# Optimization experiments

Measured on AMD Instinct MI355X. Metric: run time of the kernel, lower is better.

## Reference

```python
import jax, jax.numpy as jnp
import numpy as np

D_MODEL = 128
NHEAD = 8
NLAYERS = 6
LAYER_NAMES = ['self', 'cross', 'self', 'cross', 'self', 'cross']
TEMPERATURE = 5.0
EPS = 1e-6


def _pos_encoding(x):
    # Sinusoidal 1D position encoding along the width axis. x: [N, H, W, C]
    C, W = x.shape[-1], x.shape[2]
    pos = jnp.arange(W, dtype=x.dtype)[:, None]                      # [W,1]
    div = jnp.exp(jnp.arange(0, C, 2, dtype=x.dtype) * (-np.log(10000.0) / C))
    pe = jnp.zeros((W, C), x.dtype)
    pe = pe.at[:, 0::2].set(jnp.sin(pos * div))
    pe = pe.at[:, 1::2].set(jnp.cos(pos * div))
    return x + pe[None, None]                                        # broadcast over N,H


def _linear_attention(q, k, v):
    # q,k,v: [N, H, W, nhead, dim]; kernelized linear attention along W
    Q = jax.nn.elu(q) + 1.0
    K = jax.nn.elu(k) + 1.0
    v_len = v.shape[2]
    V = v / v_len
    KV = jnp.einsum('nhsed,nhsev->nhedv', K, V)                      # [N,H,e,d,d]
    Z = 1.0 / (jnp.einsum('nhled,nhed->nhle', Q, K.sum(axis=2)) + EPS)
    return jnp.einsum('nhled,nhedv,nhle->nhlev', Q, KV, Z) * v_len


def _layer_norm(x, g, b):
    m = x.mean(-1, keepdims=True)
    v = jnp.mean((x - m) ** 2, -1, keepdims=True)
    return (x - m) / jnp.sqrt(v + 1e-5) * g + b


def _encoder_layer(x, source, Wq, Wk, Wv, Wm, W1, W2, g1, b1, g2, b2):
    x = _pos_encoding(x)
    source = _pos_encoding(source)
    bs, h, w, c = x.shape
    e, d = NHEAD, c // NHEAD
    q = (x @ Wq).reshape(bs, h, w, e, d)
    k = (source @ Wk).reshape(bs, h, w, e, d)
    v = (source @ Wv).reshape(bs, h, w, e, d)
    msg = _linear_attention(q, k, v).reshape(bs, h, w, c) @ Wm
    msg = _layer_norm(msg, g1, b1)
    msg = jnp.concatenate([x, msg], axis=-1)                         # [N,H,W,2C]
    msg = jax.nn.relu(msg @ W1) @ W2
    msg = _layer_norm(msg, g2, b2)
    return x + msg


def _forward(feat0, feat1, Wq, Wk, Wv, Wm, W1, W2, g1, b1, g2, b2):
    feat0 = feat0.transpose(0, 2, 3, 1)                              # [N,H,W,C]
    feat1 = feat1.transpose(0, 2, 3, 1)
    for i, name in enumerate(LAYER_NAMES):
        p = (Wq[i], Wk[i], Wv[i], Wm[i], W1[i], W2[i], g1[i], b1[i], g2[i], b2[i])
        if name == 'self':
            feat0 = _encoder_layer(feat0, feat0, *p)
            feat1 = _encoder_layer(feat1, feat1, *p)
        else:  # cross: sequential update (feat1 sees updated feat0), as in torch source
            feat0 = _encoder_layer(feat0, feat1, *p)
            feat1 = _encoder_layer(feat1, feat0, *p)
    w = feat0.shape[2]
    attn_mask = jnp.where(jnp.triu(jnp.ones((w, w), bool), 1), -jnp.inf, 0.0)
    attn_mask = attn_mask[None, None].astype(feat0.dtype)
    scale = feat0.shape[-1] ** 0.5
    sim = jnp.einsum('ntwc,ntlc->ntwl', feat0 / scale, feat1 / scale) / TEMPERATURE
    return sim + attn_mask


def setup_inputs() -> dict:
    key = jax.random.key(0)
    ks = jax.random.split(key, 12)
    N, C, H, W = 2, D_MODEL, 64, 640
    L, D = NLAYERS, D_MODEL
    s = 1.0 / np.sqrt(D)
    s2 = 1.0 / np.sqrt(2 * D)
    return {
        'feat0': jax.random.normal(ks[0], (N, C, H, W), jnp.float32),
        'feat1': jax.random.normal(ks[1], (N, C, H, W), jnp.float32),
        'Wq': jax.random.normal(ks[2], (L, D, D), jnp.float32) * s,
        'Wk': jax.random.normal(ks[3], (L, D, D), jnp.float32) * s,
        'Wv': jax.random.normal(ks[4], (L, D, D), jnp.float32) * s,
        'Wm': jax.random.normal(ks[5], (L, D, D), jnp.float32) * s,
        'W1': jax.random.normal(ks[6], (L, 2 * D, 2 * D), jnp.float32) * s2,
        'W2': jax.random.normal(ks[7], (L, 2 * D, D), jnp.float32) * s2,
        'g1': jnp.ones((L, D), jnp.float32),
        'b1': jnp.zeros((L, D), jnp.float32),
        'g2': jnp.ones((L, D), jnp.float32),
        'b2': jnp.zeros((L, D), jnp.float32),
    }


def reference(feat0, feat1, Wq, Wk, Wv, Wm, W1, W2, g1, b1, g2, b2):
    return _forward(feat0, feat1, Wq, Wk, Wv, Wm, W1, W2, g1, b1, g2, b2)
```

## Files before the change

### kernel.cpp

```cpp
#include <hip/hip_runtime.h>
#include <cmath>
#include <math.h>

#define TOK 81920
#define WDIM 640

typedef __attribute__((ext_vector_type(8))) short short8v;
typedef __attribute__((ext_vector_type(4))) float f32x4;

__device__ __forceinline__ short f2bf(float f) {
  union { float f; unsigned u; } x; x.f = f;
  unsigned r = (x.u + 0x7fffu + ((x.u >> 16) & 1u)) >> 16;
  return (short)r;
}
__device__ __forceinline__ float bf2f(short s) {
  union { unsigned u; float f; } x; x.u = ((unsigned)(unsigned short)s) << 16;
  return x.f;
}

__global__ __launch_bounds__(256) void pe_kernel(float* __restrict__ pe) {
  int id = blockIdx.x * 256 + threadIdx.x;
  if (id >= WDIM * 128) return;
  int w = id >> 7;
  int c = id & 127;
  float i2 = (float)(c & 126);
  float freq = expf(i2 * -0.071955784156063941f);
  float ang = (float)w * freq;
  pe[id] = (c & 1) ? cosf(ang) : sinf(ang);
}

__global__ __launch_bounds__(256) void tr_kernel(const float* __restrict__ in0,
                                                 const float* __restrict__ in1,
                                                 short* __restrict__ x0,
                                                 short* __restrict__ x1) {
  __shared__ float t[32][33];
  int w0 = blockIdx.x * 32;
  int c0 = blockIdx.y * 32;
  int z = blockIdx.z;
  int feat = z >> 7;
  int nh = z & 127;
  int n = nh >> 6, h = nh & 63;
  const float* in = feat ? in1 : in0;
  short* out = feat ? x1 : x0;
  int tx = threadIdx.x & 31, ty = threadIdx.x >> 5;
  const float* ip = in + ((n * 128 + c0) * 64 + h) * 640 + w0;
#pragma unroll
  for (int i = 0; i < 32; i += 8)
    t[ty + i][tx] = ip[(ty + i) * (64 * 640) + tx];
  __syncthreads();
  short* op = out + ((size_t)(n * 64 + h) * 640 + w0) * 128 + c0;
#pragma unroll
  for (int i = 0; i < 32; i += 8)
    op[(size_t)(ty + i) * 128 + tx] = f2bf(t[tx][ty + i]);
}

__global__ __launch_bounds__(256) void wprep_kernel(
    const float* __restrict__ Wq, const float* __restrict__ Wk,
    const float* __restrict__ Wv, const float* __restrict__ Wm,
    const float* __restrict__ W1, const float* __restrict__ W2,
    short* __restrict__ BT) {
  int id = blockIdx.x * 256 + threadIdx.x;
  if (id >= 6 * 163840) return;
  int layer = id / 163840;
  int r = id % 163840;
  float v;
  if (r < 65536) {
    int seg = r >> 14;
    int rr = r & 16383;
    int n = rr >> 7, k = rr & 127;
    const float* W = seg == 0 ? Wq : seg == 1 ? Wk : seg == 2 ? Wv : Wm;
    v = W[layer * 16384 + k * 128 + n];
  } else if (r < 131072) {
    int rr = r - 65536;
    int n = rr >> 8, k = rr & 255;
    v = W1[layer * 65536 + k * 256 + n];
  } else {
    int rr = r - 131072;
    int n = rr >> 8, k = rr & 255;
    v = W2[layer * 32768 + k * 128 + n];
  }
  BT[id] = f2bf(v);
}

__device__ __forceinline__ void load_af(const short* __restrict__ A,
                                        const float* __restrict__ pe,
                                        int bm, int wr, int l15, int lk,
                                        short8v af[4][4]) {
  const int wbase = bm % WDIM;
#pragma unroll
  for (int mf = 0; mf < 4; ++mf) {
    const int rl = wr * 64 + mf * 16 + l15;
    const short* ar = A + (size_t)(bm + rl) * 128;
    const float* pr = pe + (size_t)(wbase + rl) * 128;
#pragma unroll
    for (int ks = 0; ks < 4; ++ks) {
      const int kloc = ks * 32 + lk * 8;
      short8v xa = *(const short8v*)(ar + kloc);
      f32x4 p0 = *(const f32x4*)(pr + kloc);
      f32x4 p1 = *(const f32x4*)(pr + kloc + 4);
      short8v o;
      o[0] = f2bf(bf2f(xa[0]) + p0[0]); o[1] = f2bf(bf2f(xa[1]) + p0[1]);
      o[2] = f2bf(bf2f(xa[2]) + p0[2]); o[3] = f2bf(bf2f(xa[3]) + p0[3]);
      o[4] = f2bf(bf2f(xa[4]) + p1[0]); o[5] = f2bf(bf2f(xa[5]) + p1[1]);
      o[6] = f2bf(bf2f(xa[6]) + p1[2]); o[7] = f2bf(bf2f(xa[7]) + p1[3]);
      af[ks][mf] = o;
    }
  }
}

__device__ __forceinline__ void proj_pass(const short8v af[4][4],
                                          const short* __restrict__ WT,
                                          int bm, int wr, int wc, int l15, int lk,
                                          short* __restrict__ out) {
  f32x4 acc[4][4] = {};
#pragma unroll
  for (int ks = 0; ks < 4; ++ks) {
    const int kloc = ks * 32 + lk * 8;
    short8v bfr[4];
#pragma unroll
    for (int nf = 0; nf < 4; ++nf)
      bfr[nf] = *(const short8v*)&WT[(size_t)(wc * 64 + nf * 16 + l15) * 128 + kloc];
#pragma unroll
    for (int mf = 0; mf < 4; ++mf)
#pragma unroll
      for (int nf = 0; nf < 4; ++nf)
        acc[mf][nf] = __builtin_amdgcn_mfma_f32_16x16x32_bf16(
            af[ks][mf], bfr[nf], acc[mf][nf], 0, 0, 0);
  }
#pragma unroll
  for (int mf = 0; mf < 4; ++mf)
#pragma unroll
    for (int nf = 0; nf < 4; ++nf) {
      const int colL = wc * 64 + nf * 16 + l15;
#pragma unroll
      for (int r = 0; r < 4; ++r) {
        const int row = bm + wr * 64 + mf * 16 + lk * 4 + r;
        out[(size_t)row * 128 + colL] = f2bf(acc[mf][nf][r]);
      }
    }
}

__global__ __launch_bounds__(256) void qkv_self_kernel(
    const short* __restrict__ x0, const short* __restrict__ x1,
    const float* __restrict__ pe,
    const short* __restrict__ wqT, const short* __restrict__ wkT,
    const short* __restrict__ wvT,
    short* q0, short* k0, short* v0, short* q1, short* k1, short* v1) {
  const int tid = threadIdx.x, lane = tid & 63, wid = tid >> 6;
  const int wr = wid >> 1, wc = wid & 1;
  const int bm = blockIdx.x * 128;
  const int l15 = lane & 15, lk = lane >> 4;
  const int z = blockIdx.z;
  const short* A = z ? x1 : x0;
  short8v af[4][4];
  load_af(A, pe, bm, wr, l15, lk, af);
  proj_pass(af, wqT, bm, wr, wc, l15, lk, z ? q1 : q0);
  proj_pass(af, wkT, bm, wr, wc, l15, lk, z ? k1 : k0);
  proj_pass(af, wvT, bm, wr, wc, l15, lk, z ? v1 : v0);
}

__global__ __launch_bounds__(256) void qkv_cross_kernel(
    const short* __restrict__ xq, const short* __restrict__ xs,
    const float* __restrict__ pe,
    const short* __restrict__ wqT, const short* __restrict__ wkT,
    const short* __restrict__ wvT,
    short* qb, short* kb, short* vb) {
  const int tid = threadIdx.x, lane = tid & 63, wid = tid >> 6;
  const int wr = wid >> 1, wc = wid & 1;
  const int bm = blockIdx.x * 128;
  const int l15 = lane & 15, lk = lane >> 4;
  short8v af[4][4];
  if (blockIdx.y == 0) {
    load_af(xq, pe, bm, wr, l15, lk, af);
    proj_pass(af, wqT, bm, wr, wc, l15, lk, qb);
  } else {
    load_af(xs, pe, bm, wr, l15, lk, af);
    proj_pass(af, wkT, bm, wr, wc, l15, lk, kb);
    proj_pass(af, wvT, bm, wr, wc, l15, lk, vb);
  }
}

template <int NSC>
__global__ __launch_bounds__(256) void kv_kernel(
    const short* __restrict__ k0, const short* __restrict__ v0,
    const short* __restrict__ k1, const short* __restrict__ v1,
    float* __restrict__ kvp) {
  const int bid = blockIdx.x;
  const int sc = bid % NSC;
  const int e = bid / NSC;
  const int strip = sc / 5, chunk = sc % 5;
  const short* kb = (strip >= 128) ? k1 : k0;
  const short* vb = (strip >= 128) ? v1 : v0;
  const int nh = strip & 127;
  const size_t base = (size_t)nh * (640 * 128) + (size_t)chunk * (128 * 128) + e * 16;
  __shared__ float Ks[128][16];
  __shared__ float Vs[128][16];
  const int tid = threadIdx.x;
  const int srow = tid >> 1, shalf = (tid & 1) * 8;
  short8v k8 = *(const short8v*)&kb[base + (size_t)srow * 128 + shalf];
  short8v v8 = *(const short8v*)&vb[base + (size_t)srow * 128 + shalf];
#pragma unroll
  for (int j = 0; j < 8; ++j) {
    float kr = bf2f(k8[j]);
    Ks[srow][shalf + j] = kr > 0.f ? kr + 1.f : __expf(kr);
    Vs[srow][shalf + j] = bf2f(v8[j]);
  }
  __syncthreads();
  const int d = tid >> 4, vv = tid & 15;
  float kv = 0.f, ks = 0.f;
#pragma unroll 8
  for (int sl = 0; sl < 128; ++sl) {
    float kk = Ks[sl][d];
    kv = fmaf(kk, Vs[sl][vv], kv);
    ks += kk;
  }
  float* out = kvp + ((size_t)(strip * 8 + e) * 5 + chunk) * 272;
  out[d * 16 + vv] = kv;
  if (vv == 0) out[256 + d] = ks;
}

template <int DUAL>
__global__ __launch_bounds__(256) void apply_wm_kernel(
    short* q0, short* q1, const float* __restrict__ kvp,
    const short* __restrict__ wmT,
    const float* __restrict__ g, const float* __restrict__ b) {
  const int bid = blockIdx.x;
  const int strip = bid / 10, lc = bid % 10;
  __shared__ float KV8[8][16][17];
  __shared__ float KS8[8][16];
  __shared__ short oS[64][136];
  const int tid = threadIdx.x;
  for (int idx = tid; idx < 8 * 272; idx += 256) {
    int e = idx / 272, r = idx - e * 272;
    const float* p = kvp + ((size_t)(strip * 8 + e) * 5) * 272 + r;
    float s = ((p[0] + p[272]) + (p[544] + p[816])) + p[1088];
    if (r < 256) KV8[e][r >> 4][r & 15] = s;
    else         KS8[e][r - 256] = s;
  }
  __syncthreads();
  short* qb = (DUAL && strip >= 128) ? q1 : q0;
  const int nh = strip & 127;
  const int lrow = tid >> 2;
  const int row = lc * 64 + lrow;
  const int cb = (tid & 3) * 32;
  short* qp = qb + (size_t)nh * (640 * 128) + (size_t)row * 128 + cb;
  short8v qv0 = *(const short8v*)(qp);
  short8v qv1 = *(const short8v*)(qp + 8);
  short8v qv2 = *(const short8v*)(qp + 16);
  short8v qv3 = *(const short8v*)(qp + 24);
  float qe[32];
#pragma unroll
  for (int j = 0; j < 8; ++j) {
    float a = bf2f(qv0[j]); qe[j]      = a > 0.f ? a + 1.f : __expf(a);
    float c1 = bf2f(qv1[j]); qe[8 + j]  = c1 > 0.f ? c1 + 1.f : __expf(c1);
    float c2 = bf2f(qv2[j]); qe[16 + j] = c2 > 0.f ? c2 + 1.f : __expf(c2);
    float c3 = bf2f(qv3[j]); qe[24 + j] = c3 > 0.f ? c3 + 1.f : __expf(c3);
  }
  short res[32];
#pragma unroll
  for (int h = 0; h < 2; ++h) {
    const int e = (cb >> 4) + h;
    const float* Q = qe + h * 16;
    float dz = 0.f;
#pragma unroll
    for (int dd = 0; dd < 16; ++dd) dz = fmaf(Q[dd], KS8[e][dd], dz);
    const float zi = 1.f / (dz + 1e-6f);
#pragma unroll
    for (int vv = 0; vv < 16; ++vv) {
      float o = 0.f;
#pragma unroll
      for (int dd = 0; dd < 16; ++dd) o = fmaf(Q[dd], KV8[e][dd][vv], o);
      res[h * 16 + vv] = f2bf(o * zi);
    }
  }
  short8v w0, w1, w2, w3;
#pragma unroll
  for (int j = 0; j < 8; ++j) {
    w0[j] = res[j]; w1[j] = res[8 + j]; w2[j] = res[16 + j]; w3[j] = res[24 + j];
  }
  *(short8v*)&oS[lrow][cb]      = w0;
  *(short8v*)&oS[lrow][cb + 8]  = w1;
  *(short8v*)&oS[lrow][cb + 16] = w2;
  *(short8v*)&oS[lrow][cb + 24] = w3;
  __syncthreads();
  const int lane = tid & 63, w = tid >> 6;
  const int l15 = lane & 15, lk = lane >> 4;
  f32x4 acc[8] = {};
#pragma unroll
  for (int ks = 0; ks < 4; ++ks) {
    const int kloc = ks * 32 + lk * 8;
    short8v afr = *(const short8v*)&oS[w * 16 + l15][kloc];
    short8v bfr[8];
#pragma unroll
    for (int nf = 0; nf < 8; ++nf)
      bfr[nf] = *(const short8v*)&wmT[(size_t)(nf * 16 + l15) * 128 + kloc];
#pragma unroll
    for (int nf = 0; nf < 8; ++nf)
      acc[nf] = __builtin_amdgcn_mfma_f32_16x16x32_bf16(afr, bfr[nf], acc[nf], 0, 0, 0);
  }
  float gv[8], bv[8];
#pragma unroll
  for (int nf = 0; nf < 8; ++nf) { gv[nf] = g[nf * 16 + l15]; bv[nf] = b[nf * 16 + l15]; }
#pragma unroll
  for (int r = 0; r < 4; ++r) {
    float s = 0.f, qq = 0.f;
#pragma unroll
    for (int nf = 0; nf < 8; ++nf) {
      s += acc[nf][r];
      qq = fmaf(acc[nf][r], acc[nf][r], qq);
    }
#pragma unroll
    for (int off = 1; off < 16; off <<= 1) {
      s += __shfl_xor(s, off);
      qq += __shfl_xor(qq, off);
    }
    float mean = s * (1.f / 128.f);
    float var = qq * (1.f / 128.f) - mean * mean;
    float rstd = rsqrtf(var + 1e-5f);
    const int grow = lc * 64 + w * 16 + lk * 4 + r;
    short* mp = qb + (size_t)nh * (640 * 128) + (size_t)grow * 128;
#pragma unroll
    for (int nf = 0; nf < 8; ++nf)
      mp[nf * 16 + l15] = f2bf((acc[nf][r] - mean) * rstd * gv[nf] + bv[nf]);
  }
}

__global__ __launch_bounds__(256) void w1_kernel(
    const short* __restrict__ xA, const short* __restrict__ xB,
    const short* __restrict__ mA, const short* __restrict__ mB,
    const float* __restrict__ pe, const short* __restrict__ w1T,
    short* h0A, short* h1A, short* h0B, short* h1B) {
  const int z = blockIdx.z;
  const short* x = z ? xB : xA;
  const short* m = z ? mB : mA;
  short* h0 = z ? h0B : h0A;
  short* h1 = z ? h1B : h1A;
  const int tid = threadIdx.x, lane = tid & 63, wid = tid >> 6;
  const int wr = wid >> 1, wc = wid & 1;
  const int bm = blockIdx.x * 128;
  const int l15 = lane & 15, lk = lane >> 4;
  const int wbase = bm % WDIM;
  for (int p = 0; p < 2; ++p) {
    f32x4 acc[4][4] = {};
#pragma unroll
    for (int ks = 0; ks < 8; ++ks) {
      const int kloc = ks * 32 + lk * 8;
      short8v bfr[4], afr[4];
#pragma unroll
      for (int nf = 0; nf < 4; ++nf)
        bfr[nf] = *(const short8v*)&w1T[(size_t)(p * 128 + wc * 64 + nf * 16 + l15) * 256 + kloc];
      if (ks < 4) {
#pragma unroll
        for (int mf = 0; mf < 4; ++mf) {
          const int rl = wr * 64 + mf * 16 + l15;
          short8v xa = *(const short8v*)(x + (size_t)(bm + rl) * 128 + kloc);
          const float* pr = pe + (size_t)(wbase + rl) * 128 + kloc;
          f32x4 p0 = *(const f32x4*)pr;
          f32x4 p1 = *(const f32x4*)(pr + 4);
          short8v ov;
          ov[0] = f2bf(bf2f(xa[0]) + p0[0]); ov[1] = f2bf(bf2f(xa[1]) + p0[1]);
          ov[2] = f2bf(bf2f(xa[2]) + p0[2]); ov[3] = f2bf(bf2f(xa[3]) + p0[3]);
          ov[4] = f2bf(bf2f(xa[4]) + p1[0]); ov[5] = f2bf(bf2f(xa[5]) + p1[1]);
          ov[6] = f2bf(bf2f(xa[6]) + p1[2]); ov[7] = f2bf(bf2f(xa[7]) + p1[3]);
          afr[mf] = ov;
        }
      } else {
#pragma unroll
        for (int mf = 0; mf < 4; ++mf)
          afr[mf] = *(const short8v*)&m[(size_t)(bm + wr * 64 + mf * 16 + l15) * 128 + kloc - 128];
      }
#pragma unroll
      for (int mf = 0; mf < 4; ++mf)
#pragma unroll
        for (int nf = 0; nf < 4; ++nf)
          acc[mf][nf] = __builtin_amdgcn_mfma_f32_16x16x32_bf16(
              afr[mf], bfr[nf], acc[mf][nf], 0, 0, 0);
    }
    short* h = p ? h1 : h0;
#pragma unroll
    for (int mf = 0; mf < 4; ++mf)
#pragma unroll
      for (int nf = 0; nf < 4; ++nf) {
        const int colL = wc * 64 + nf * 16 + l15;
#pragma unroll
        for (int r = 0; r < 4; ++r) {
          const int row = bm + wr * 64 + mf * 16 + lk * 4 + r;
          h[(size_t)row * 128 + colL] = f2bf(fmaxf(acc[mf][nf][r], 0.f));
        }
      }
  }
}

__global__ __launch_bounds__(256) void w2_ln_kernel(
    const short* __restrict__ h0A, const short* __restrict__ h1A,
    const short* __restrict__ h0B, const short* __restrict__ h1B,
    const short* __restrict__ w2T, short* xA, short* xB,
    const float* __restrict__ pe, const float* __restrict__ g,
    const float* __restrict__ b) {
  const int z = blockIdx.z;
  const short* h0 = z ? h0B : h0A;
  const short* h1 = z ? h1B : h1A;
  short* x = z ? xB : xA;
  __shared__ float lds_s[2][128];
  __shared__ float lds_q[2][128];
  const int tid = threadIdx.x, lane = tid & 63, wid = tid >> 6;
  const int wr = wid >> 1, wc = wid & 1;
  const int bm = blockIdx.x * 128;
  const int l15 = lane & 15, lk = lane >> 4;
  const int wbase = bm % WDIM;
  f32x4 acc[4][4] = {};
#pragma unroll
  for (int ks = 0; ks < 8; ++ks) {
    const int kloc = ks * 32 + lk * 8;
    const short* hp = (ks < 4) ? h0 : h1;
    const int kl = (ks < 4) ? kloc : kloc - 128;
    short8v bfr[4], afr[4];
#pragma unroll
    for (int nf = 0; nf < 4; ++nf)
      bfr[nf] = *(const short8v*)&w2T[(size_t)(wc * 64 + nf * 16 + l15) * 256 + kloc];
#pragma unroll
    for (int mf = 0; mf < 4; ++mf)
      afr[mf] = *(const short8v*)&hp[(size_t)(bm + wr * 64 + mf * 16 + l15) * 128 + kl];
#pragma unroll
    for (int mf = 0; mf < 4; ++mf)
#pragma unroll
      for (int nf = 0; nf < 4; ++nf)
        acc[mf][nf] = __builtin_amdgcn_mfma_f32_16x16x32_bf16(
            afr[mf], bfr[nf], acc[mf][nf], 0, 0, 0);
  }
#pragma unroll
  for (int mf = 0; mf < 4; ++mf)
#pragma unroll
    for (int r = 0; r < 4; ++r) {
      float s = acc[mf][0][r] + acc[mf][1][r] + acc[mf][2][r] + acc[mf][3][r];
      float qq = acc[mf][0][r] * acc[mf][0][r] + acc[mf][1][r] * acc[mf][1][r]
               + acc[mf][2][r] * acc[mf][2][r] + acc[mf][3][r] * acc[mf][3][r];
#pragma unroll
      for (int off = 1; off < 16; off <<= 1) {
        s += __shfl_xor(s, off);
        qq += __shfl_xor(qq, off);
      }
      if (l15 == 0) {
        int rl = wr * 64 + mf * 16 + lk * 4 + r;
        lds_s[wc][rl] = s;
        lds_q[wc][rl] = qq;
      }
    }
  __syncthreads();
  float gv[4], bv[4];
#pragma unroll
  for (int nf = 0; nf < 4; ++nf) {
    int c = wc * 64 + nf * 16 + l15;
    gv[nf] = g[c]; bv[nf] = b[c];
  }
#pragma unroll
  for (int mf = 0; mf < 4; ++mf)
#pragma unroll
    for (int r = 0; r < 4; ++r) {
      int rl = wr * 64 + mf * 16 + lk * 4 + r;
      float mean = (lds_s[0][rl] + lds_s[1][rl]) * (1.f / 128.f);
      float var = (lds_q[0][rl] + lds_q[1][rl]) * (1.f / 128.f) - mean * mean;
      float rstd = rsqrtf(var + 1e-5f);
      int row = bm + rl;
#pragma unroll
      for (int nf = 0; nf < 4; ++nf) {
        int col = wc * 64 + nf * 16 + l15;
        float ln = (acc[mf][nf][r] - mean) * rstd * gv[nf] + bv[nf];
        size_t xi = (size_t)row * 128 + col;
        float xv = bf2f(x[xi]) + pe[(size_t)(wbase + rl) * 128 + col] + ln;
        x[xi] = f2bf(xv);
      }
    }
}

__global__ __launch_bounds__(256) void sim_mfma(const short* __restrict__ f0,
                                                const short* __restrict__ f1,
                                                float* __restrict__ out) {
  const int fid = (blockIdx.z * 5 + blockIdx.y) * 5 + blockIdx.x;
  const int c8 = fid & 7, kk_ = fid >> 3;
  const int nt = c8 * 16 + kk_ / 25;
  const int r2 = kk_ % 25;
  const int bw = (r2 % 5) * 128;
  const int bl = (r2 / 5) * 128;
  const int tid = threadIdx.x;
  const int lane = tid & 63;
  const int wid = tid >> 6;
  const int wr = wid >> 1, wc = wid & 1;
  const short* __restrict__ A = f0 + (size_t)nt * 640 * 128;
  const short* __restrict__ B = f1 + (size_t)nt * 640 * 128;
  const int l15 = lane & 15;
  const int lk = lane >> 4;
  f32x4 acc[4][4] = {};
#pragma unroll
  for (int ks = 0; ks < 4; ++ks) {
    const int kloc = ks * 32 + lk * 8;
    short8v afr[4], bfr[4];
#pragma unroll
    for (int mf = 0; mf < 4; ++mf)
      afr[mf] = *(const short8v*)&A[(size_t)(bw + wr * 64 + mf * 16 + l15) * 128 + kloc];
#pragma unroll
    for (int nf = 0; nf < 4; ++nf)
      bfr[nf] = *(const short8v*)&B[(size_t)(bl + wc * 64 + nf * 16 + l15) * 128 + kloc];
#pragma unroll
    for (int mf = 0; mf < 4; ++mf)
#pragma unroll
      for (int nf = 0; nf < 4; ++nf)
        acc[mf][nf] = __builtin_amdgcn_mfma_f32_16x16x32_bf16(
            afr[mf], bfr[nf], acc[mf][nf], 0, 0, 0);
  }
#pragma unroll
  for (int mf = 0; mf < 4; ++mf)
#pragma unroll
    for (int nf = 0; nf < 4; ++nf) {
      const int l = bl + wc * 64 + nf * 16 + l15;
#pragma unroll
      for (int r = 0; r < 4; ++r) {
        const int w = bw + wr * 64 + mf * 16 + lk * 4 + r;
        float v = acc[mf][nf][r] * (1.f / 640.f);
        if (l > w) v = -1e30f;
        out[((size_t)nt * 640 + w) * 640 + l] = v;
      }
    }
}

extern "C" void kernel_launch(void* const* d_in, const int* in_sizes, int n_in,
                              void* d_out, int out_size, void* d_ws, size_t ws_size,
                              hipStream_t stream) {
  (void)in_sizes; (void)n_in; (void)out_size; (void)ws_size;
  const float* feat0 = (const float*)d_in[0];
  const float* feat1 = (const float*)d_in[1];
  const float* Wq = (const float*)d_in[2];
  const float* Wk = (const float*)d_in[3];
  const float* Wv = (const float*)d_in[4];
  const float* Wm = (const float*)d_in[5];
  const float* W1 = (const float*)d_in[6];
  const float* W2 = (const float*)d_in[7];
  const float* g1 = (const float*)d_in[8];
  const float* b1 = (const float*)d_in[9];
  const float* g2 = (const float*)d_in[10];
  const float* b2 = (const float*)d_in[11];

  float* wsf = (float*)d_ws;
  const size_t U = (size_t)TOK * 128;
  float* pe = wsf;
  short* x0 = (short*)(wsf + 81920);
  short* x1 = x0 + U;
  short* q0 = x1 + U;
  short* k0 = q0 + U;
  short* v0 = k0 + U;
  short* q1 = v0 + U;
  short* k1 = q1 + U;
  short* v1 = k1 + U;
  short* bt = v1 + U;
  float* kvp = (float*)(bt + 983040);

  dim3 blk(256);
  pe_kernel<<<dim3(320), blk, 0, stream>>>(pe);
  tr_kernel<<<dim3(20, 4, 256), blk, 0, stream>>>(feat0, feat1, x0, x1);
  wprep_kernel<<<dim3((6 * 163840 + 255) / 256), blk, 0, stream>>>(
      Wq, Wk, Wv, Wm, W1, W2, bt);

  const int NB = TOK / 128;
  for (int i = 0; i < 6; ++i) {
    const short* bt_i = bt + (size_t)i * 163840;
    const short* wqT = bt_i;
    const short* wkT = bt_i + 16384;
    const short* wvT = bt_i + 32768;
    const short* wmT = bt_i + 49152;
    const short* w1T = bt_i + 65536;
    const short* w2T = bt_i + 131072;
    const float* g1_i = g1 + i * 128;
    const float* b1_i = b1 + i * 128;
    const float* g2_i = g2 + i * 128;
    const float* b2_i = b2 + i * 128;
    if ((i & 1) == 0) {
      qkv_self_kernel<<<dim3(NB, 1, 2), blk, 0, stream>>>(
          x0, x1, pe, wqT, wkT, wvT, q0, k0, v0, q1, k1, v1);
      kv_kernel<1280><<<dim3(8 * 1280), blk, 0, stream>>>(k0, v0, k1, v1, kvp);
      apply_wm_kernel<1><<<dim3(2560), blk, 0, stream>>>(q0, q1, kvp, wmT, g1_i, b1_i);
      w1_kernel<<<dim3(NB, 1, 2), blk, 0, stream>>>(
          x0, x1, q0, q1, pe, w1T, k0, v0, k1, v1);
      w2_ln_kernel<<<dim3(NB, 1, 2), blk, 0, stream>>>(
          k0, v0, k1, v1, w2T, x0, x1, pe, g2_i, b2_i);
    } else {
      qkv_cross_kernel<<<dim3(NB, 2), blk, 0, stream>>>(
          x0, x1, pe, wqT, wkT, wvT, q0, k0, v0);
      kv_kernel<640><<<dim3(8 * 640), blk, 0, stream>>>(k0, v0, k0, v0, kvp);
      apply_wm_kernel<0><<<dim3(1280), blk, 0, stream>>>(q0, q0, kvp, wmT, g1_i, b1_i);
      w1_kernel<<<dim3(NB, 1, 1), blk, 0, stream>>>(
          x0, x0, q0, q0, pe, w1T, k0, v0, k0, v0);
      w2_ln_kernel<<<dim3(NB, 1, 1), blk, 0, stream>>>(
          k0, v0, k0, v0, w2T, x0, x0, pe, g2_i, b2_i);

      qkv_cross_kernel<<<dim3(NB, 2), blk, 0, stream>>>(
          x1, x0, pe, wqT, wkT, wvT, q0, k0, v0);
      kv_kernel<640><<<dim3(8 * 640), blk, 0, stream>>>(k0, v0, k0, v0, kvp);
      apply_wm_kernel<0><<<dim3(1280), blk, 0, stream>>>(q0, q0, kvp, wmT, g1_i, b1_i);
      w1_kernel<<<dim3(NB, 1, 1), blk, 0, stream>>>(
          x1, x1, q0, q0, pe, w1T, k0, v0, k0, v0);
      w2_ln_kernel<<<dim3(NB, 1, 1), blk, 0, stream>>>(
          k0, v0, k0, v0, w2T, x1, x1, pe, g2_i, b2_i);
    }
  }
  sim_mfma<<<dim3(5, 5, 128), blk, 0, stream>>>(x0, x1, (float*)d_out);
}
```

Baseline: 2.767 ms.

## Stage GEMM epilogues through LDS for coalesced 16-byte global stores

Swaps the MFMA operand order so each lane holds four contiguous output columns, packs them into short4 writes to a padded LDS tile, then writes the tile to global memory with coalesced 16-byte stores. This applies to the QKV projections, the attention-output/Wm LayerNorm epilogue, the W1 ReLU epilogue and the W2 LayerNorm-residual epilogue. It replaces scattered 2-byte strided global stores and simplifies the LayerNorm reductions to two cross-lane shuffles. In exchange it adds LDS usage and extra barriers per block, which may reduce occupancy.

```diff
diff --git a/kernel.cpp b/kernel.cpp
--- a/kernel.cpp
+++ b/kernel.cpp
@@ -6,6 +6,7 @@
 #define WDIM 640
 
 typedef __attribute__((ext_vector_type(8))) short short8v;
+typedef __attribute__((ext_vector_type(4))) short short4v;
 typedef __attribute__((ext_vector_type(4))) float f32x4;
 
 __device__ __forceinline__ short f2bf(float f) {
@@ -108,10 +109,10 @@
   }
 }
 
-__device__ __forceinline__ void proj_pass(const short8v af[4][4],
-                                          const short* __restrict__ WT,
-                                          int bm, int wr, int wc, int l15, int lk,
-                                          short* __restrict__ out) {
+__device__ __forceinline__ void proj_pass_T(const short8v af[4][4],
+                                            const short* __restrict__ WT,
+                                            int wr, int wc, int l15, int lk,
+                                            short (*tS)[136]) {
   f32x4 acc[4][4] = {};
 #pragma unroll
   for (int ks = 0; ks < 4; ++ks) {
@@ -125,19 +126,28 @@
 #pragma unroll
       for (int nf = 0; nf < 4; ++nf)
         acc[mf][nf] = __builtin_amdgcn_mfma_f32_16x16x32_bf16(
-            af[ks][mf], bfr[nf], acc[mf][nf], 0, 0, 0);
+            bfr[nf], af[ks][mf], acc[mf][nf], 0, 0, 0);
   }
 #pragma unroll
   for (int mf = 0; mf < 4; ++mf)
 #pragma unroll
     for (int nf = 0; nf < 4; ++nf) {
-      const int colL = wc * 64 + nf * 16 + l15;
-#pragma unroll
-      for (int r = 0; r < 4; ++r) {
-        const int row = bm + wr * 64 + mf * 16 + lk * 4 + r;
-        out[(size_t)row * 128 + colL] = f2bf(acc[mf][nf][r]);
-      }
-    }
+      short4v p;
+      p[0] = f2bf(acc[mf][nf][0]); p[1] = f2bf(acc[mf][nf][1]);
+      p[2] = f2bf(acc[mf][nf][2]); p[3] = f2bf(acc[mf][nf][3]);
+      *(short4v*)&tS[wr * 64 + mf * 16 + l15][wc * 64 + nf * 16 + lk * 4] = p;
+    }
+}
+
+__device__ __forceinline__ void tile_out(const short (*tS)[136], int bm, int tid,
+                                         short* __restrict__ out) {
+#pragma unroll
+  for (int it = 0; it < 8; ++it) {
+    int u = it * 256 + tid;
+    int row = u >> 4, seg = u & 15;
+    *(short8v*)&out[(size_t)(bm + row) * 128 + seg * 8] =
+        *(const short8v*)&tS[row][seg * 8];
+  }
 }
 
 __global__ __launch_bounds__(256) void qkv_self_kernel(
@@ -146,6 +156,7 @@
     const short* __restrict__ wqT, const short* __restrict__ wkT,
     const short* __restrict__ wvT,
     short* q0, short* k0, short* v0, short* q1, short* k1, short* v1) {
+  __shared__ short tS[128][136];
   const int tid = threadIdx.x, lane = tid & 63, wid = tid >> 6;
   const int wr = wid >> 1, wc = wid & 1;
   const int bm = blockIdx.x * 128;
@@ -154,9 +165,17 @@
   const short* A = z ? x1 : x0;
   short8v af[4][4];
   load_af(A, pe, bm, wr, l15, lk, af);
-  proj_pass(af, wqT, bm, wr, wc, l15, lk, z ? q1 : q0);
-  proj_pass(af, wkT, bm, wr, wc, l15, lk, z ? k1 : k0);
-  proj_pass(af, wvT, bm, wr, wc, l15, lk, z ? v1 : v0);
+  proj_pass_T(af, wqT, wr, wc, l15, lk, tS);
+  __syncthreads();
+  tile_out(tS, bm, tid, z ? q1 : q0);
+  __syncthreads();
+  proj_pass_T(af, wkT, wr, wc, l15, lk, tS);
+  __syncthreads();
+  tile_out(tS, bm, tid, z ? k1 : k0);
+  __syncthreads();
+  proj_pass_T(af, wvT, wr, wc, l15, lk, tS);
+  __syncthreads();
+  tile_out(tS, bm, tid, z ? v1 : v0);
 }
 
 __global__ __launch_bounds__(256) void qkv_cross_kernel(
@@ -165,6 +184,7 @@
     const short* __restrict__ wqT, const short* __restrict__ wkT,
     const short* __restrict__ wvT,
     short* qb, short* kb, short* vb) {
+  __shared__ short tS[128][136];
   const int tid = threadIdx.x, lane = tid & 63, wid = tid >> 6;
   const int wr = wid >> 1, wc = wid & 1;
   const int bm = blockIdx.x * 128;
@@ -172,11 +192,18 @@
   short8v af[4][4];
   if (blockIdx.y == 0) {
     load_af(xq, pe, bm, wr, l15, lk, af);
-    proj_pass(af, wqT, bm, wr, wc, l15, lk, qb);
+    proj_pass_T(af, wqT, wr, wc, l15, lk, tS);
+    __syncthreads();
+    tile_out(tS, bm, tid, qb);
   } else {
     load_af(xs, pe, bm, wr, l15, lk, af);
-    proj_pass(af, wkT, bm, wr, wc, l15, lk, kb);
-    proj_pass(af, wvT, bm, wr, wc, l15, lk, vb);
+    proj_pass_T(af, wkT, wr, wc, l15, lk, tS);
+    __syncthreads();
+    tile_out(tS, bm, tid, kb);
+    __syncthreads();
+    proj_pass_T(af, wvT, wr, wc, l15, lk, tS);
+    __syncthreads();
+    tile_out(tS, bm, tid, vb);
   }
 }
 
@@ -283,45 +310,51 @@
   *(short8v*)&oS[lrow][cb + 16] = w2;
   *(short8v*)&oS[lrow][cb + 24] = w3;
   __syncthreads();
-  const int lane = tid & 63, w = tid >> 6;
+  const int lane = tid & 63, wv = tid >> 6;
   const int l15 = lane & 15, lk = lane >> 4;
   f32x4 acc[8] = {};
 #pragma unroll
   for (int ks = 0; ks < 4; ++ks) {
     const int kloc = ks * 32 + lk * 8;
-    short8v afr = *(const short8v*)&oS[w * 16 + l15][kloc];
+    short8v afr = *(const short8v*)&oS[wv * 16 + l15][kloc];
     short8v bfr[8];
 #pragma unroll
     for (int nf = 0; nf < 8; ++nf)
       bfr[nf] = *(const short8v*)&wmT[(size_t)(nf * 16 + l15) * 128 + kloc];
 #pragma unroll
     for (int nf = 0; nf < 8; ++nf)
-      acc[nf] = __builtin_amdgcn_mfma_f32_16x16x32_bf16(afr, bfr[nf], acc[nf], 0, 0, 0);
-  }
-  float gv[8], bv[8];
-#pragma unroll
-  for (int nf = 0; nf < 8; ++nf) { gv[nf] = g[nf * 16 + l15]; bv[nf] = b[nf * 16 + l15]; }
-#pragma unroll
-  for (int r = 0; r < 4; ++r) {
-    float s = 0.f, qq = 0.f;
-#pragma unroll
-    for (int nf = 0; nf < 8; ++nf) {
+      acc[nf] = __builtin_amdgcn_mfma_f32_16x16x32_bf16(bfr[nf], afr, acc[nf], 0, 0, 0);
+  }
+  float s = 0.f, qq = 0.f;
+#pragma unroll
+  for (int nf = 0; nf < 8; ++nf)
+#pragma unroll
+    for (int r = 0; r < 4; ++r) {
       s += acc[nf][r];
       qq = fmaf(acc[nf][r], acc[nf][r], qq);
     }
-#pragma unroll
-    for (int off = 1; off < 16; off <<= 1) {
-      s += __shfl_xor(s, off);
-      qq += __shfl_xor(qq, off);
-    }
-    float mean = s * (1.f / 128.f);
-    float var = qq * (1.f / 128.f) - mean * mean;
-    float rstd = rsqrtf(var + 1e-5f);
-    const int grow = lc * 64 + w * 16 + lk * 4 + r;
-    short* mp = qb + (size_t)nh * (640 * 128) + (size_t)grow * 128;
-#pragma unroll
-    for (int nf = 0; nf < 8; ++nf)
-      mp[nf * 16 + l15] = f2bf((acc[nf][r] - mean) * rstd * gv[nf] + bv[nf]);
+  s += __shfl_xor(s, 16);  qq += __shfl_xor(qq, 16);
+  s += __shfl_xor(s, 32);  qq += __shfl_xor(qq, 32);
+  float mean = s * (1.f / 128.f);
+  float var = qq * (1.f / 128.f) - mean * mean;
+  float rstd = rsqrtf(var + 1e-5f);
+#pragma unroll
+  for (int nf = 0; nf < 8; ++nf) {
+    f32x4 g4 = *(const f32x4*)&g[nf * 16 + lk * 4];
+    f32x4 b4 = *(const f32x4*)&b[nf * 16 + lk * 4];
+    short4v p;
+#pragma unroll
+    for (int r = 0; r < 4; ++r)
+      p[r] = f2bf((acc[nf][r] - mean) * rstd * g4[r] + b4[r]);
+    *(short4v*)&oS[wv * 16 + l15][nf * 16 + lk * 4] = p;
+  }
+  __syncthreads();
+  short* mp = qb + (size_t)nh * (640 * 128) + (size_t)(lc * 64) * 128;
+#pragma unroll
+  for (int it = 0; it < 4; ++it) {
+    int u = it * 256 + tid;
+    int rw = u >> 4, seg = u & 15;
+    *(short8v*)&mp[(size_t)rw * 128 + seg * 8] = *(const short8v*)&oS[rw][seg * 8];
   }
 }
 
@@ -330,6 +363,7 @@
     const short* __restrict__ mA, const short* __restrict__ mB,
     const float* __restrict__ pe, const short* __restrict__ w1T,
     short* h0A, short* h1A, short* h0B, short* h1B) {
+  __shared__ short tS[128][136];
   const int z = blockIdx.z;
   const short* x = z ? xB : xA;
   const short* m = z ? mB : mA;
@@ -374,20 +408,21 @@
 #pragma unroll
         for (int nf = 0; nf < 4; ++nf)
           acc[mf][nf] = __builtin_amdgcn_mfma_f32_16x16x32_bf16(
-              afr[mf], bfr[nf], acc[mf][nf], 0, 0, 0);
-    }
-    short* h = p ? h1 : h0;
+              bfr[nf], afr[mf], acc[mf][nf], 0, 0, 0);
+    }
 #pragma unroll
     for (int mf = 0; mf < 4; ++mf)
 #pragma unroll
       for (int nf = 0; nf < 4; ++nf) {
-        const int colL = wc * 64 + nf * 16 + l15;
-#pragma unroll
-        for (int r = 0; r < 4; ++r) {
-          const int row = bm + wr * 64 + mf * 16 + lk * 4 + r;
-          h[(size_t)row * 128 + colL] = f2bf(fmaxf(acc[mf][nf][r], 0.f));
-        }
+        short4v pk;
+#pragma unroll
+        for (int r = 0; r < 4; ++r)
+          pk[r] = f2bf(fmaxf(acc[mf][nf][r], 0.f));
+        *(short4v*)&tS[wr * 64 + mf * 16 + l15][wc * 64 + nf * 16 + lk * 4] = pk;
       }
+    __syncthreads();
+    tile_out(tS, bm, tid, p ? h1 : h0);
+    __syncthreads();
   }
 }
 
@@ -397,12 +432,13 @@
     const short* __restrict__ w2T, short* xA, short* xB,
     const float* __restrict__ pe, const float* __restrict__ g,
     const float* __restrict__ b) {
+  __shared__ short tS[128][136];
+  __shared__ float lds_s[2][128];
+  __shared__ float lds_q[2][128];
   const int z = blockIdx.z;
   const short* h0 = z ? h0B : h0A;
   const short* h1 = z ? h1B : h1A;
   short* x = z ? xB : xA;
-  __shared__ float lds_s[2][128];
-  __shared__ float lds_q[2][128];
   const int tid = threadIdx.x, lane = tid & 63, wid = tid >> 6;
   const int wr = wid >> 1, wc = wid & 1;
   const int bm = blockIdx.x * 128;
@@ -426,51 +462,66 @@
 #pragma unroll
       for (int nf = 0; nf < 4; ++nf)
         acc[mf][nf] = __builtin_amdgcn_mfma_f32_16x16x32_bf16(
-            afr[mf], bfr[nf], acc[mf][nf], 0, 0, 0);
-  }
-#pragma unroll
-  for (int mf = 0; mf < 4; ++mf)
-#pragma unroll
-    for (int r = 0; r < 4; ++r) {
-      float s = acc[mf][0][r] + acc[mf][1][r] + acc[mf][2][r] + acc[mf][3][r];
-      float qq = acc[mf][0][r] * acc[mf][0][r] + acc[mf][1][r] * acc[mf][1][r]
-               + acc[mf][2][r] * acc[mf][2][r] + acc[mf][3][r] * acc[mf][3][r];
-#pragma unroll
-      for (int off = 1; off < 16; off <<= 1) {
-        s += __shfl_xor(s, off);
-        qq += __shfl_xor(qq, off);
+            bfr[nf], afr[mf], acc[mf][nf], 0, 0, 0);
+  }
+#pragma unroll
+  for (int mf = 0; mf < 4; ++mf) {
+    float s = 0.f, qq = 0.f;
+#pragma unroll
+    for (int nf = 0; nf < 4; ++nf)
+#pragma unroll
+      for (int r = 0; r < 4; ++r) {
+        s += acc[mf][nf][r];
+        qq = fmaf(acc[mf][nf][r], acc[mf][nf][r], qq);
       }
-      if (l15 == 0) {
-        int rl = wr * 64 + mf * 16 + lk * 4 + r;
-        lds_s[wc][rl] = s;
-        lds_q[wc][rl] = qq;
-      }
-    }
-  __syncthreads();
-  float gv[4], bv[4];
-#pragma unroll
-  for (int nf = 0; nf < 4; ++nf) {
-    int c = wc * 64 + nf * 16 + l15;
-    gv[nf] = g[c]; bv[nf] = b[c];
-  }
-#pragma unroll
-  for (int mf = 0; mf < 4; ++mf)
-#pragma unroll
-    for (int r = 0; r < 4; ++r) {
-      int rl = wr * 64 + mf * 16 + lk * 4 + r;
-      float mean = (lds_s[0][rl] + lds_s[1][rl]) * (1.f / 128.f);
-      float var = (lds_q[0][rl] + lds_q[1][rl]) * (1.f / 128.f) - mean * mean;
-      float rstd = rsqrtf(var + 1e-5f);
-      int row = bm + rl;
-#pragma unroll
-      for (int nf = 0; nf < 4; ++nf) {
-        int col = wc * 64 + nf * 16 + l15;
-        float ln = (acc[mf][nf][r] - mean) * rstd * gv[nf] + bv[nf];
-        size_t xi = (size_t)row * 128 + col;
-        float xv = bf2f(x[xi]) + pe[(size_t)(wbase + rl) * 128 + col] + ln;
-        x[xi] = f2bf(xv);
-      }
-    }
+    s += __shfl_xor(s, 16);  qq += __shfl_xor(qq, 16);
+    s += __shfl_xor(s, 32);  qq += __shfl_xor(qq, 32);
+    if (lk == 0) {
+      int rl = wr * 64 + mf * 16 + l15;
+      lds_s[wc][rl] = s;
+      lds_q[wc][rl] = qq;
+    }
+  }
+  __syncthreads();
+#pragma unroll
+  for (int mf = 0; mf < 4; ++mf) {
+    int rl = wr * 64 + mf * 16 + l15;
+    float mean = (lds_s[0][rl] + lds_s[1][rl]) * (1.f / 128.f);
+    float var = (lds_q[0][rl] + lds_q[1][rl]) * (1.f / 128.f) - mean * mean;
+    float rstd = rsqrtf(var + 1e-5f);
+#pragma unroll
+    for (int nf = 0; nf < 4; ++nf) {
+      f32x4 g4 = *(const f32x4*)&g[wc * 64 + nf * 16 + lk * 4];
+      f32x4 b4 = *(const f32x4*)&b[wc * 64 + nf * 16 + lk * 4];
+      short4v pk;
+#pragma unroll
+      for (int r = 0; r < 4; ++r)
+        pk[r] = f2bf((acc[mf][nf][r] - mean) * rstd * g4[r] + b4[r]);
+      *(short4v*)&tS[rl][wc * 64 + nf * 16 + lk * 4] = pk;
+    }
+  }
+  __syncthreads();
+#pragma unroll
+  for (int it = 0; it < 8; ++it) {
+    int u = it * 256 + tid;
+    int row = u >> 4, seg = u & 15;
+    size_t xi = (size_t)(bm + row) * 128 + seg * 8;
+    short8v xv8 = *(const short8v*)&x[xi];
+    short8v t8 = *(const short8v*)&tS[row][seg * 8];
+    const float* pr = pe + (size_t)(wbase + row) * 128 + seg * 8;
+    f32x4 p0 = *(const f32x4*)pr;
+    f32x4 p1 = *(const f32x4*)(pr + 4);
+    short8v o8;
+    o8[0] = f2bf(bf2f(xv8[0]) + p0[0] + bf2f(t8[0]));
+    o8[1] = f2bf(bf2f(xv8[1]) + p0[1] + bf2f(t8[1]));
+    o8[2] = f2bf(bf2f(xv8[2]) + p0[2] + bf2f(t8[2]));
+    o8[3] = f2bf(bf2f(xv8[3]) + p0[3] + bf2f(t8[3]));
+    o8[4] = f2bf(bf2f(xv8[4]) + p1[0] + bf2f(t8[4]));
+    o8[5] = f2bf(bf2f(xv8[5]) + p1[1] + bf2f(t8[5]));
+    o8[6] = f2bf(bf2f(xv8[6]) + p1[2] + bf2f(t8[6]));
+    o8[7] = f2bf(bf2f(xv8[7]) + p1[3] + bf2f(t8[7]));
+    *(short8v*)&x[xi] = o8;
+  }
 }
 
 __global__ __launch_bounds__(256) void sim_mfma(const short* __restrict__ f0,
```

Result: faster. 2.487 ms (median of 2 runs) (-10.1%).
